# Optimization experiments

Measured on AMD Instinct MI355X. Metric: run time of the kernel, lower is better.

The kernel has to match this reference:

```python
import jax, jax.numpy as jnp
import numpy as np

DIM, HEADS, HEAD_DIM = 1024, 16, 64
B, S = 2, 1024
LAMBDA = 4.0
EPS = 1e-6


def setup_inputs() -> dict:
    key = jax.random.key(0)
    ks = jax.random.split(key, 7)
    sc = 1.0 / np.sqrt(DIM)
    return {
        "x": jax.random.normal(ks[0], (B, S, DIM), jnp.float32),
        "qkv_w": jax.random.normal(ks[1], (3 * DIM, DIM), jnp.float32) * sc,
        "qkv_b": jax.random.normal(ks[2], (3 * DIM,), jnp.float32) * 0.01,
        "proj_w": jax.random.normal(ks[3], (DIM, DIM), jnp.float32) * sc,
        "proj_b": jax.random.normal(ks[4], (DIM,), jnp.float32) * 0.01,
        "dwc_w": jax.random.normal(ks[5], (DIM, 1, 3), jnp.float32) * 0.3,
        "dwc_b": jax.random.normal(ks[6], (DIM,), jnp.float32) * 0.01,
    }


def _l1_dist(q, k):
    # q,k: [B,H,S,Dh] -> pairwise L1 distance [B,H,S,S].
    # Accumulate over head_dim with a (rematerialized) scan so we never
    # materialize the [B,H,S,S,Dh] broadcast tensor.
    qT = jnp.moveaxis(q, -1, 0)  # [Dh,B,H,S]
    kT = jnp.moveaxis(k, -1, 0)

    def step(acc, qk):
        qd, kd = qk  # [B,H,S]
        return acc + jnp.abs(qd[..., :, None] - kd[..., None, :]), None

    init = jnp.zeros(q.shape[:-1] + (k.shape[-2],), q.dtype)
    dist, _ = jax.lax.scan(jax.checkpoint(step), init, (qT, kT))
    return dist


def reference(x, qkv_w, qkv_b, proj_w, proj_b, dwc_w, dwc_b):
    Bq, Sq, C = x.shape
    # qkv projection -> q,k,v each [B,H,S,Dh]
    qkv = (x @ qkv_w.T + qkv_b).reshape(Bq, Sq, 3, HEADS, HEAD_DIM)
    qkv = jnp.transpose(qkv, (2, 0, 3, 1, 4))
    q, k, v = qkv[0], qkv[1], qkv[2]

    # exact Laplacian (L1-distance) kernel attention, row-normalized
    dist = _l1_dist(q, k)                       # [B,H,S,S]
    kern = jnp.exp(-LAMBDA * dist / HEAD_DIM)   # mean-L1 scaling
    attn = kern / (jnp.sum(kern, axis=-1, keepdims=True) + EPS)
    global_attn = jnp.einsum("bhij,bhjd->bhid", attn, v)

    # depthwise conv1d local branch on v (channel order = head-major)
    v1d = jnp.transpose(v, (0, 1, 3, 2)).reshape(Bq, C, Sq)  # [B,C,S]
    local = jax.lax.conv_general_dilated(
        v1d, dwc_w, window_strides=(1,), padding=((1, 1),),
        feature_group_count=C, dimension_numbers=("NCH", "OIH", "NCH"))
    local = local + dwc_b[None, :, None]
    local = jnp.transpose(local.reshape(Bq, HEADS, HEAD_DIM, Sq), (0, 1, 3, 2))

    y = global_attn + local                      # [B,H,S,Dh]
    y = jnp.transpose(y, (0, 2, 1, 3)).reshape(Bq, Sq, C)
    return y @ proj_w.T + proj_b
```

## Files before the change

### kernel.cpp

```cpp
#include <hip/hip_runtime.h>

#define DIMC 1024
#define HEADS 16
#define HD 64
#define BATCH 2
#define SEQ 1024
#define NQKV 3072

typedef _Float16 f16;
typedef _Float16 half8 __attribute__((ext_vector_type(8)));
typedef _Float16 half4v __attribute__((ext_vector_type(4)));
typedef float floatx4 __attribute__((ext_vector_type(4)));

__device__ __forceinline__ void gld16(const void* g, void* l) {
  __builtin_amdgcn_global_load_lds((const __attribute__((address_space(1))) void*)g,
                                   (__attribute__((address_space(3))) void*)l, 16, 0, 0);
}

__device__ __forceinline__ unsigned sadU8(unsigned a, unsigned b, unsigned c) {
#if __has_builtin(__builtin_amdgcn_sad_u8)
  return __builtin_amdgcn_sad_u8(a, b, c);
#else
  unsigned d;
  asm("v_sad_u8 %0, %1, %2, %3" : "=v"(d) : "v"(a), "v"(b), "v"(c));
  return d;
#endif
}

__global__ __launch_bounds__(256) void cvt_kernel(
    const float* __restrict__ x, const float* __restrict__ wq, const float* __restrict__ wp,
    f16* __restrict__ x16, f16* __restrict__ wq16, f16* __restrict__ wp16)
{
  long long bid = blockIdx.x;
  const float* src; f16* dst; long long base;
  if (bid < 2048)            { src = x;  dst = x16;  base = bid; }
  else if (bid < 2048+3072)  { src = wq; dst = wq16; base = bid - 2048; }
  else                       { src = wp; dst = wp16; base = bid - (2048+3072); }
  long long i = base*256 + threadIdx.x;
  float4 v = ((const float4*)src)[i];
  half4v h; h[0]=(f16)v.x; h[1]=(f16)v.y; h[2]=(f16)v.z; h[3]=(f16)v.w;
  *(half4v*)(dst + i*4) = h;
}

template<int TM, int TN, int MODE>
__global__ __launch_bounds__(256, 4) void gemm_kernel(
    const f16* __restrict__ A, const f16* __restrict__ Bw, const float* __restrict__ bias,
    unsigned char* __restrict__ q8, unsigned char* __restrict__ k8, f16* __restrict__ vT,
    float* __restrict__ outp, int K)
{
  constexpr int MT = TM / 32;
  constexpr int NT = TN / 32;
  __shared__ f16 As[TM*64];
  __shared__ f16 Bs[TN*64];
  const int tid = threadIdx.x;
  const int wave = tid >> 6, lane = tid & 63;
  const int lq = lane >> 4, li = lane & 15;
  const int m0 = blockIdx.y * TM, n0 = blockIdx.x * TN;
  const int wm = (wave & 1) * (TM/2), wn = (wave >> 1) * (TN/2);
  floatx4 acc[MT][NT] = {};

  const int kIters = K / 64;
  for (int kt = 0; kt < kIters; ++kt) {
    __syncthreads();
#pragma unroll
    for (int r = 0; r < TM/32; ++r) {
      int slot = r*256 + tid;
      int row = slot >> 3, c = slot & 7, sc = c ^ (row & 7);
      gld16(A + (size_t)(m0+row)*K + kt*64 + sc*8, As + slot*8);
    }
#pragma unroll
    for (int r = 0; r < TN/32; ++r) {
      int slot = r*256 + tid;
      int row = slot >> 3, c = slot & 7, sc = c ^ (row & 7);
      gld16(Bw + (size_t)(n0+row)*K + kt*64 + sc*8, Bs + slot*8);
    }
    __syncthreads();
#pragma unroll
    for (int ks = 0; ks < 2; ++ks) {
      half8 af[MT], bf[NT];
      int kc = ks*4 + lq;
#pragma unroll
      for (int t = 0; t < MT; ++t) {
        int am = wm + t*16 + li;
        af[t] = *(const half8*)&As[am*64 + (kc ^ (am & 7))*8];
      }
#pragma unroll
      for (int t = 0; t < NT; ++t) {
        int bn = wn + t*16 + li;
        bf[t] = *(const half8*)&Bs[bn*64 + (kc ^ (bn & 7))*8];
      }
#pragma unroll
      for (int mt = 0; mt < MT; ++mt)
#pragma unroll
        for (int nt = 0; nt < NT; ++nt)
          acc[mt][nt] = __builtin_amdgcn_mfma_f32_16x16x32_f16(af[mt], bf[nt], acc[mt][nt], 0, 0, 0);
    }
  }

#pragma unroll
  for (int mt = 0; mt < MT; ++mt) {
#pragma unroll
    for (int nt = 0; nt < NT; ++nt) {
      int f = n0 + wn + nt*16 + li;
      float bb = bias[f];
      if (MODE == 0) {
        int which = f >> 10, cc = f & 1023, h = cc >> 6, d = cc & 63;
        int t0 = m0 + wm + mt*16 + lq*4;
        int b = t0 >> 10, s0 = t0 & 1023;
        if (which == 2) {
          half4v hv;
#pragma unroll
          for (int r = 0; r < 4; ++r) hv[r] = (f16)(acc[mt][nt][r] + bb);
          *(half4v*)&vT[((size_t)((b*HEADS + h)*HD + d))*SEQ + s0] = hv;
        } else {
          unsigned char* dst = (which == 0) ? q8 : k8;
#pragma unroll
          for (int r = 0; r < 4; ++r) {
            float v = acc[mt][nt][r] + bb;
            int u = (int)floorf(v * 16.0f + 128.5f);
            u = u < 0 ? 0 : (u > 255 ? 255 : u);
            dst[((size_t)((b*HEADS + h)*SEQ + s0 + r))*HD + d] = (unsigned char)u;
          }
        }
      } else {
#pragma unroll
        for (int r = 0; r < 4; ++r) {
          int t = m0 + wm + mt*16 + lq*4 + r;
          outp[(size_t)t*DIMC + f] = acc[mt][nt][r] + bb;
        }
      }
    }
  }
}

__global__ __launch_bounds__(256, 4) void attn_kernel(
    const unsigned char* __restrict__ q8g, const unsigned char* __restrict__ k8g,
    const f16* __restrict__ vTg, const float* __restrict__ dwcw, const float* __restrict__ dwcb,
    f16* __restrict__ y16)
{
  __shared__ unsigned char q8s[32*64];
  __shared__ unsigned char k8s[128*64];
  __shared__ f16 sfrag[8*64*8];
  __shared__ float rspart[32*16];
  __shared__ float rowsumS[32];
  __shared__ f16 vconv[64*34];

  const int tid = threadIdx.x;
  const int bh = blockIdx.y;
  const int i0 = blockIdx.x * 32;
  const int lane = tid & 63, wave = tid >> 6;
  const int lq = lane >> 4, li = lane & 15;
  const int iL = tid & 15, jt = tid >> 4;
  const int ksj = jt >> 2, qj = jt & 3;
  const int mtb = wave & 1, ntb = wave >> 1;

  if (wave < 2)
    gld16(q8g + ((size_t)bh*SEQ + i0)*HD + tid*16, q8s + tid*16);

  {
    int d = tid >> 2, part = tid & 3;
    const f16* vrow = vTg + ((size_t)(bh*HD) + d)*SEQ;
#pragma unroll
    for (int e = 0; e < 9; ++e) {
      int ss = part*9 + e;
      if (ss < 34) {
        int s = i0 - 1 + ss;
        vconv[d*34 + ss] = (s >= 0 && s < SEQ) ? vrow[s] : (f16)0.0f;
      }
    }
  }
  __syncthreads();

  unsigned qr[2][16];
#pragma unroll
  for (int n = 0; n < 2; ++n)
#pragma unroll
    for (int c4 = 0; c4 < 4; ++c4) {
      uint4 t = *(const uint4*)&q8s[(iL + n*16)*64 + c4*16];
      qr[n][c4*4+0] = t.x; qr[n][c4*4+1] = t.y; qr[n][c4*4+2] = t.z; qr[n][c4*4+3] = t.w;
    }

  float rs[2] = {0.f, 0.f};
  floatx4 pacc[2] = {};

  for (int jb = 0; jb < 8; ++jb) {
    const int j0 = jb * 128;
    __syncthreads();
#pragma unroll
    for (int r = 0; r < 2; ++r) {
      int slot = r*256 + tid;
      gld16(k8g + ((size_t)bh*SEQ + j0)*HD + slot*16, k8s + slot*16);
    }
    __syncthreads();

    unsigned sacc[2][8] = {};
#pragma unroll
    for (int c4 = 0; c4 < 4; ++c4) {
      uint4 kk[8];
#pragma unroll
      for (int jj = 0; jj < 8; ++jj)
        kk[jj] = *(const uint4*)&k8s[(jt*8 + jj)*64 + c4*16];
#pragma unroll
      for (int n = 0; n < 2; ++n)
#pragma unroll
        for (int jj = 0; jj < 8; ++jj) {
          sacc[n][jj] = sadU8(qr[n][c4*4+0], kk[jj].x, sacc[n][jj]);
          sacc[n][jj] = sadU8(qr[n][c4*4+1], kk[jj].y, sacc[n][jj]);
          sacc[n][jj] = sadU8(qr[n][c4*4+2], kk[jj].z, sacc[n][jj]);
          sacc[n][jj] = sadU8(qr[n][c4*4+3], kk[jj].w, sacc[n][jj]);
        }
    }
#pragma unroll
    for (int n = 0; n < 2; ++n) {
      half8 sv;
#pragma unroll
      for (int jj = 0; jj < 8; ++jj) {
        float sf = exp2f(-0.0056355275f * (float)sacc[n][jj]);
        rs[n] += sf;
        sv[jj] = (f16)sf;
      }
      *(half8*)&sfrag[((n*4 + ksj)*64 + qj*16 + iL)*8] = sv;
    }
    __syncthreads();

#pragma unroll
    for (int ks = 0; ks < 4; ++ks) {
      half8 a = *(const half8*)&sfrag[((mtb*4 + ks)*64 + lane)*8];
#pragma unroll
      for (int nt = 0; nt < 2; ++nt) {
        int d = (ntb*2 + nt)*16 + li;
        half8 bfr = *(const half8*)(vTg + ((size_t)(bh*HD) + d)*SEQ + j0 + (ks*4 + lq)*8);
        pacc[nt] = __builtin_amdgcn_mfma_f32_16x16x32_f16(a, bfr, pacc[nt], 0, 0, 0);
      }
    }
  }

#pragma unroll
  for (int n = 0; n < 2; ++n) rspart[(iL + n*16)*16 + jt] = rs[n];
  __syncthreads();
  if (tid < 32) {
    float s = 0.f;
#pragma unroll
    for (int t = 0; t < 16; ++t) s += rspart[tid*16 + t];
    rowsumS[tid] = s + 1e-6f;
  }
  __syncthreads();

  const int b = bh >> 4, h = bh & 15;
#pragma unroll
  for (int nt = 0; nt < 2; ++nt) {
    int d = (ntb*2 + nt)*16 + li;
    int c = h*64 + d;
    float w0 = dwcw[c*3+0], w1 = dwcw[c*3+1], w2 = dwcw[c*3+2], cb = dwcb[c];
#pragma unroll
    for (int r = 0; r < 4; ++r) {
      int ii = mtb*16 + lq*4 + r;
      float val = pacc[nt][r] / rowsumS[ii];
      val += w0*(float)vconv[d*34 + ii] + w1*(float)vconv[d*34 + ii + 1]
           + w2*(float)vconv[d*34 + ii + 2] + cb;
      int s = i0 + ii;
      y16[((size_t)(b*SEQ + s))*DIMC + c] = (f16)val;
    }
  }
}

extern "C" void kernel_launch(void* const* d_in, const int* in_sizes, int n_in,
                              void* d_out, int out_size, void* d_ws, size_t ws_size,
                              hipStream_t stream) {
  const float* x      = (const float*)d_in[0];
  const float* qkv_w  = (const float*)d_in[1];
  const float* qkv_b  = (const float*)d_in[2];
  const float* proj_w = (const float*)d_in[3];
  const float* proj_b = (const float*)d_in[4];
  const float* dwc_w  = (const float*)d_in[5];
  const float* dwc_b  = (const float*)d_in[6];
  float* out = (float*)d_out;

  char* ws = (char*)d_ws;
  f16* x16  = (f16*)(ws);
  f16* wq16 = (f16*)(ws + (4ll<<20));
  f16* wp16 = (f16*)(ws + (10ll<<20));
  unsigned char* q8 = (unsigned char*)(ws + (12ll<<20));
  unsigned char* k8 = (unsigned char*)(ws + (14ll<<20));
  f16* vT   = (f16*)(ws + (16ll<<20));
  f16* y16  = (f16*)(ws + (20ll<<20));

  cvt_kernel<<<6144, 256, 0, stream>>>(x, qkv_w, proj_w, x16, wq16, wp16);
  gemm_kernel<64,128,0><<<dim3(24, 32), 256, 0, stream>>>(x16, wq16, qkv_b, q8, k8, vT, nullptr, DIMC);
  attn_kernel<<<dim3(32, 32), 256, 0, stream>>>(q8, k8, vT, dwc_w, dwc_b, y16);
  gemm_kernel<64,64,1><<<dim3(16, 32), 256, 0, stream>>>(y16, wp16, proj_b, nullptr, nullptr, nullptr, out, DIMC);
}
```

Baseline: 162.0 us.

## Double-buffer K tiles in attention, reshape SAD tiling, widen GEMM K-step

The attention kernel now double-buffers the K tile in shared memory, so the load of the next 128-key block is issued before computing on the current one. It also changes the thread-to-work mapping so each thread does 4 query rows by 4 keys, with XOR swizzling on the K and score fragments to reduce LDS bank conflicts. V fragments are prefetched into registers before the SAD loop, and row sums are reduced with wave shuffles instead of a 16-way LDS reduction. Both GEMMs move to a K step of 128 with generalized swizzling, and both kernels drop to 3 blocks per CU. The larger LDS footprint and higher register use may reduce occupancy.

Result: slower. 168.1 us (+3.8%).

```diff
diff --git a/kernel.cpp b/kernel.cpp
--- a/kernel.cpp
+++ b/kernel.cpp
@@ -42,16 +42,17 @@
   *(half4v*)(dst + i*4) = h;
 }
 
-template<int TM, int TN, int MODE>
-__global__ __launch_bounds__(256, 4) void gemm_kernel(
+template<int TM, int TN, int BK, int MODE>
+__global__ __launch_bounds__(256, 3) void gemm_kernel(
     const f16* __restrict__ A, const f16* __restrict__ Bw, const float* __restrict__ bias,
     unsigned char* __restrict__ q8, unsigned char* __restrict__ k8, f16* __restrict__ vT,
     float* __restrict__ outp, int K)
 {
   constexpr int MT = TM / 32;
   constexpr int NT = TN / 32;
-  __shared__ f16 As[TM*64];
-  __shared__ f16 Bs[TN*64];
+  constexpr int G  = BK / 8;
+  __shared__ f16 As[TM*BK];
+  __shared__ f16 Bs[TN*BK];
   const int tid = threadIdx.x;
   const int wave = tid >> 6, lane = tid & 63;
   const int lq = lane >> 4, li = lane & 15;
@@ -59,35 +60,35 @@
   const int wm = (wave & 1) * (TM/2), wn = (wave >> 1) * (TN/2);
   floatx4 acc[MT][NT] = {};
 
-  const int kIters = K / 64;
+  const int kIters = K / BK;
   for (int kt = 0; kt < kIters; ++kt) {
     __syncthreads();
 #pragma unroll
-    for (int r = 0; r < TM/32; ++r) {
+    for (int r = 0; r < TM*BK/2048; ++r) {
       int slot = r*256 + tid;
-      int row = slot >> 3, c = slot & 7, sc = c ^ (row & 7);
-      gld16(A + (size_t)(m0+row)*K + kt*64 + sc*8, As + slot*8);
-    }
-#pragma unroll
-    for (int r = 0; r < TN/32; ++r) {
+      int row = slot / G, c = slot % G, g = c ^ (row & (G-1));
+      gld16(A + (size_t)(m0+row)*K + kt*BK + g*8, As + slot*8);
+    }
+#pragma unroll
+    for (int r = 0; r < TN*BK/2048; ++r) {
       int slot = r*256 + tid;
-      int row = slot >> 3, c = slot & 7, sc = c ^ (row & 7);
-      gld16(Bw + (size_t)(n0+row)*K + kt*64 + sc*8, Bs + slot*8);
+      int row = slot / G, c = slot % G, g = c ^ (row & (G-1));
+      gld16(Bw + (size_t)(n0+row)*K + kt*BK + g*8, Bs + slot*8);
     }
     __syncthreads();
 #pragma unroll
-    for (int ks = 0; ks < 2; ++ks) {
+    for (int ks = 0; ks < BK/32; ++ks) {
       half8 af[MT], bf[NT];
       int kc = ks*4 + lq;
 #pragma unroll
       for (int t = 0; t < MT; ++t) {
         int am = wm + t*16 + li;
-        af[t] = *(const half8*)&As[am*64 + (kc ^ (am & 7))*8];
+        af[t] = *(const half8*)&As[am*BK + (kc ^ (am & (G-1)))*8];
       }
 #pragma unroll
       for (int t = 0; t < NT; ++t) {
         int bn = wn + t*16 + li;
-        bf[t] = *(const half8*)&Bs[bn*64 + (kc ^ (bn & 7))*8];
+        bf[t] = *(const half8*)&Bs[bn*BK + (kc ^ (bn & (G-1)))*8];
       }
 #pragma unroll
       for (int mt = 0; mt < MT; ++mt)
@@ -133,15 +134,15 @@
   }
 }
 
-__global__ __launch_bounds__(256, 4) void attn_kernel(
+__global__ __launch_bounds__(256, 3) void attn_kernel(
     const unsigned char* __restrict__ q8g, const unsigned char* __restrict__ k8g,
     const f16* __restrict__ vTg, const float* __restrict__ dwcw, const float* __restrict__ dwcb,
     f16* __restrict__ y16)
 {
   __shared__ unsigned char q8s[32*64];
-  __shared__ unsigned char k8s[128*64];
-  __shared__ f16 sfrag[8*64*8];
-  __shared__ float rspart[32*16];
+  __shared__ unsigned char k8s[2][128*64];
+  __shared__ f16 sfrag[2][8*64*8];
+  __shared__ float rspart[32*4];
   __shared__ float rowsumS[32];
   __shared__ f16 vconv[64*34];
 
@@ -150,8 +151,9 @@
   const int i0 = blockIdx.x * 32;
   const int lane = tid & 63, wave = tid >> 6;
   const int lq = lane >> 4, li = lane & 15;
-  const int iL = tid & 15, jt = tid >> 4;
-  const int ksj = jt >> 2, qj = jt & 3;
+  const int iL = tid & 7;
+  const int jt = tid >> 3;
+  const int sub = (jt >> 1) & 3, par = jt & 1;
   const int mtb = wave & 1, ntb = wave >> 1;
 
   if (wave < 2)
@@ -169,81 +171,103 @@
       }
     }
   }
-  __syncthreads();
-
-  unsigned qr[2][16];
-#pragma unroll
-  for (int n = 0; n < 2; ++n)
-#pragma unroll
-    for (int c4 = 0; c4 < 4; ++c4) {
-      uint4 t = *(const uint4*)&q8s[(iL + n*16)*64 + c4*16];
-      qr[n][c4*4+0] = t.x; qr[n][c4*4+1] = t.y; qr[n][c4*4+2] = t.z; qr[n][c4*4+3] = t.w;
-    }
-
-  float rs[2] = {0.f, 0.f};
-  floatx4 pacc[2] = {};
-
-  for (int jb = 0; jb < 8; ++jb) {
-    const int j0 = jb * 128;
-    __syncthreads();
+
+  auto stageK = [&](int buf, int jb) {
+    const unsigned char* kg = k8g + ((size_t)bh*SEQ + jb*128)*HD;
 #pragma unroll
     for (int r = 0; r < 2; ++r) {
       int slot = r*256 + tid;
-      gld16(k8g + ((size_t)bh*SEQ + j0)*HD + slot*16, k8s + slot*16);
-    }
-    __syncthreads();
-
-    unsigned sacc[2][8] = {};
+      int row = slot >> 2, g = (slot & 3) ^ ((row >> 2) & 3);
+      gld16(kg + row*64 + g*16, k8s[buf] + slot*16);
+    }
+  };
+
+  stageK(0, 0);
+  __syncthreads();
+
+  unsigned qr[4][16];
+#pragma unroll
+  for (int n = 0; n < 4; ++n)
 #pragma unroll
     for (int c4 = 0; c4 < 4; ++c4) {
-      uint4 kk[8];
-#pragma unroll
-      for (int jj = 0; jj < 8; ++jj)
-        kk[jj] = *(const uint4*)&k8s[(jt*8 + jj)*64 + c4*16];
-#pragma unroll
-      for (int n = 0; n < 2; ++n)
-#pragma unroll
-        for (int jj = 0; jj < 8; ++jj) {
+      uint4 t = *(const uint4*)&q8s[(iL + 8*n)*64 + c4*16];
+      qr[n][c4*4+0] = t.x; qr[n][c4*4+1] = t.y; qr[n][c4*4+2] = t.z; qr[n][c4*4+3] = t.w;
+    }
+
+  float rs[4] = {0.f, 0.f, 0.f, 0.f};
+  floatx4 pacc[2] = {};
+
+  for (int jb = 0; jb < 8; ++jb) {
+    const int cur = jb & 1;
+    const int j0 = jb * 128;
+
+    if (jb < 7) stageK(cur ^ 1, jb + 1);
+
+    half8 bfr[2][4];
+#pragma unroll
+    for (int nt = 0; nt < 2; ++nt)
+#pragma unroll
+      for (int ks = 0; ks < 4; ++ks)
+        bfr[nt][ks] = *(const half8*)(vTg + ((size_t)(bh*HD) + (ntb*2+nt)*16 + li)*SEQ
+                                      + j0 + ks*32 + lq*8);
+
+    const unsigned char* kb = k8s[cur];
+
+    unsigned sacc[4][4] = {};
+#pragma unroll
+    for (int c4 = 0; c4 < 4; ++c4) {
+      uint4 kk[4];
+#pragma unroll
+      for (int jj = 0; jj < 4; ++jj)
+        kk[jj] = *(const uint4*)&kb[(jt*4 + jj)*64 + (c4 ^ (jt & 3))*16];
+#pragma unroll
+      for (int n = 0; n < 4; ++n)
+#pragma unroll
+        for (int jj = 0; jj < 4; ++jj) {
           sacc[n][jj] = sadU8(qr[n][c4*4+0], kk[jj].x, sacc[n][jj]);
           sacc[n][jj] = sadU8(qr[n][c4*4+1], kk[jj].y, sacc[n][jj]);
           sacc[n][jj] = sadU8(qr[n][c4*4+2], kk[jj].z, sacc[n][jj]);
           sacc[n][jj] = sadU8(qr[n][c4*4+3], kk[jj].w, sacc[n][jj]);
         }
     }
-#pragma unroll
-    for (int n = 0; n < 2; ++n) {
-      half8 sv;
-#pragma unroll
-      for (int jj = 0; jj < 8; ++jj) {
+
+#pragma unroll
+    for (int n = 0; n < 4; ++n) {
+      half4v sv;
+#pragma unroll
+      for (int jj = 0; jj < 4; ++jj) {
         float sf = exp2f(-0.0056355275f * (float)sacc[n][jj]);
         rs[n] += sf;
         sv[jj] = (f16)sf;
       }
-      *(half8*)&sfrag[((n*4 + ksj)*64 + qj*16 + iL)*8] = sv;
-    }
+      int frow = iL + 8*(n & 1);
+      *(half4v*)&sfrag[cur][(((n>>1)*4 + wave)*64 + sub*16 + (frow ^ (sub*2)))*8 + par*4] = sv;
+    }
+
     __syncthreads();
 
 #pragma unroll
     for (int ks = 0; ks < 4; ++ks) {
-      half8 a = *(const half8*)&sfrag[((mtb*4 + ks)*64 + lane)*8];
-#pragma unroll
-      for (int nt = 0; nt < 2; ++nt) {
-        int d = (ntb*2 + nt)*16 + li;
-        half8 bfr = *(const half8*)(vTg + ((size_t)(bh*HD) + d)*SEQ + j0 + (ks*4 + lq)*8);
-        pacc[nt] = __builtin_amdgcn_mfma_f32_16x16x32_f16(a, bfr, pacc[nt], 0, 0, 0);
-      }
-    }
-  }
-
-#pragma unroll
-  for (int n = 0; n < 2; ++n) rspart[(iL + n*16)*16 + jt] = rs[n];
+      half8 a = *(const half8*)&sfrag[cur][((mtb*4 + ks)*64 + lq*16 + (li ^ (lq*2)))*8];
+#pragma unroll
+      for (int nt = 0; nt < 2; ++nt)
+        pacc[nt] = __builtin_amdgcn_mfma_f32_16x16x32_f16(a, bfr[nt][ks], pacc[nt], 0, 0, 0);
+    }
+  }
+
+#pragma unroll
+  for (int n = 0; n < 4; ++n) {
+    rs[n] += __shfl_xor(rs[n], 8, 64);
+    rs[n] += __shfl_xor(rs[n], 16, 64);
+    rs[n] += __shfl_xor(rs[n], 32, 64);
+  }
+  if (lane < 8) {
+#pragma unroll
+    for (int n = 0; n < 4; ++n) rspart[(iL + 8*n)*4 + wave] = rs[n];
+  }
   __syncthreads();
-  if (tid < 32) {
-    float s = 0.f;
-#pragma unroll
-    for (int t = 0; t < 16; ++t) s += rspart[tid*16 + t];
-    rowsumS[tid] = s + 1e-6f;
-  }
+  if (tid < 32)
+    rowsumS[tid] = rspart[tid*4+0] + rspart[tid*4+1] + rspart[tid*4+2] + rspart[tid*4+3] + 1e-6f;
   __syncthreads();
 
   const int b = bh >> 4, h = bh & 15;
@@ -286,7 +310,7 @@
   f16* y16  = (f16*)(ws + (20ll<<20));
 
   cvt_kernel<<<6144, 256, 0, stream>>>(x, qkv_w, proj_w, x16, wq16, wp16);
-  gemm_kernel<64,128,0><<<dim3(24, 32), 256, 0, stream>>>(x16, wq16, qkv_b, q8, k8, vT, nullptr, DIMC);
+  gemm_kernel<64,128,128,0><<<dim3(24, 32), 256, 0, stream>>>(x16, wq16, qkv_b, q8, k8, vT, nullptr, DIMC);
   attn_kernel<<<dim3(32, 32), 256, 0, stream>>>(q8, k8, vT, dwc_w, dwc_b, y16);
-  gemm_kernel<64,64,1><<<dim3(16, 32), 256, 0, stream>>>(y16, wp16, proj_b, nullptr, nullptr, nullptr, out, DIMC);
-}
+  gemm_kernel<64,64,128,1><<<dim3(16, 32), 256, 0, stream>>>(y16, wp16, proj_b, nullptr, nullptr, nullptr, out, DIMC);
+}
```
